# Kernel optimization log

Hardware: AMD Instinct MI355X
Metric: run time of the kernel (lower is better)

Reference implementation:

```python
import jax, jax.numpy as jnp
import numpy as np

DIM = 512
N = 1024
DIM_HEAD = 64
HEADS = 8
BATCH = 8
SCALE = DIM_HEAD ** -0.5


def setup_inputs() -> dict:
    key = jax.random.key(0)
    ks = jax.random.split(key, 9)
    s = 0.02
    return {
        "x": jax.random.normal(ks[0], (BATCH, N, DIM), dtype=jnp.float32),
        "w_qkv": jax.random.normal(ks[1], (3 * DIM, DIM), dtype=jnp.float32) * s,
        "b_qkv": jax.random.normal(ks[2], (3 * DIM,), dtype=jnp.float32) * s,
        "wq": jax.random.normal(ks[3], (N, DIM_HEAD), dtype=jnp.float32) * s,
        "bq": jax.random.normal(ks[4], (N,), dtype=jnp.float32) * s,
        "wk": jax.random.normal(ks[5], (N, DIM_HEAD), dtype=jnp.float32) * s,
        "bk": jax.random.normal(ks[6], (N,), dtype=jnp.float32) * s,
        "w_out": jax.random.normal(ks[7], (DIM, DIM), dtype=jnp.float32) * s,
        "b_out": jax.random.normal(ks[8], (DIM,), dtype=jnp.float32) * s,
    }


def _split_heads(t):
    # [b, n, h*d] -> [b, h, n, d]
    b, n, _ = t.shape
    return t.reshape(b, n, HEADS, DIM_HEAD).transpose(0, 2, 1, 3)


def reference(x, w_qkv, b_qkv, wq, bq, wk, bk, w_out, b_out):
    # fused QKV projection: [b, n, 3*dim]
    qkv = x @ w_qkv.T + b_qkv
    qo, ko, vo = jnp.split(qkv, 3, axis=-1)
    q, k, v = _split_heads(qo), _split_heads(ko), _split_heads(vo)  # [b,h,n,d]

    # additive-attention stage 1: A = softmax(Wq(q) * scale) over last dim
    A = jax.nn.softmax((jnp.einsum('bhnd,md->bhnm', q, wq) + bq) * SCALE, axis=-1)  # [b,h,n,n]
    q_global = jnp.sum(jnp.einsum('bhnm,bhmd->bhnd', A, q), axis=-1, keepdims=True)  # [b,h,n,1]
    p = q_global * k  # [b,h,n,d]

    # stage 2
    B = jax.nn.softmax((jnp.einsum('bhnd,md->bhnm', p, wk) + bk) * SCALE, axis=-1)  # [b,h,n,n]
    k_global = jnp.sum(jnp.einsum('bhnm,bhmd->bhnd', B, p), axis=-1, keepdims=True)  # [b,h,n,1]

    u = (k_global * v).transpose(0, 2, 1, 3).reshape(x.shape[0], N, DIM)  # [b,n,dim]
    out = u @ w_out.T + b_out + qo
    return out
```

## Files before the change

kernel.cpp:

```cpp
#include <hip/hip_runtime.h>


#define SCL 0.125f
#define SCL2 0.1803368801f
typedef unsigned short u16;
typedef __attribute__((ext_vector_type(8))) short short8;
typedef __attribute__((ext_vector_type(4))) float f32x4;

#define MFMA16(a, b, c) __builtin_amdgcn_mfma_f32_16x16x32_bf16((a), (b), (c), 0, 0, 0)

__device__ __forceinline__ float bf2f(u16 u) {
    union { unsigned int i; float f; } v; v.i = ((unsigned int)u) << 16; return v.f;
}
__device__ __forceinline__ u16 f2bf(float f) {
    union { float f; unsigned int i; } v; v.f = f;
    unsigned int x = v.i;
    return (u16)((x + 0x7FFFu + ((x >> 16) & 1u)) >> 16);
}

__device__ __forceinline__ void gload16(const u16* g, u16* l) {
    __builtin_amdgcn_global_load_lds(
        (__attribute__((address_space(1))) void*)(void*)g,
        (__attribute__((address_space(3))) void*)l, 16, 0, 0);
}

__global__ __launch_bounds__(256) void conv_kernel(
    const float* __restrict__ w_qkv, const float* __restrict__ w_out,
    const float* __restrict__ wq, const float* __restrict__ wk,
    const float* __restrict__ x, u16* __restrict__ wsb)
{
    const int idx = (blockIdx.x * 256 + threadIdx.x) * 4;
    const float* src; int off;
    if      (idx < 786432)  { src = w_qkv; off = idx; }
    else if (idx < 1048576) { src = w_out; off = idx - 786432; }
    else if (idx < 1114112) { src = wq;    off = idx - 1048576; }
    else if (idx < 1179648) { src = wk;    off = idx - 1114112; }
    else                    { src = x;     off = idx - 1179648; }
    float4 v = *(const float4*)(src + off);
    ushort4 o; o.x = f2bf(v.x); o.y = f2bf(v.y); o.z = f2bf(v.z); o.w = f2bf(v.w);
    *(ushort4*)(wsb + idx) = o;
}

#define MQK 0
#define MVU 1
#define MOUT 2

template <int MODE, int NCT>
__global__ __launch_bounds__(256) void gemm_k(
    const u16* __restrict__ Ab, int lda, int acol,
    const u16* __restrict__ Wb, const float* __restrict__ bias,
    const float* __restrict__ kg, const u16* __restrict__ qkws_ro,
    u16* __restrict__ qkws, float* __restrict__ outp,
    float* __restrict__ qsout, float* __restrict__ ksout)
{
    constexpr int BN = NCT * 16;
    constexpr int CST = BN + 8;
    constexpr int ASZ = 128 * 64;
    constexpr int BSZ = BN * 64;
    constexpr int HALF = ASZ + BSZ;
    constexpr int CELEM = 128 * CST;
    constexpr int SMSZ = (2 * HALF > HALF + CELEM) ? 2 * HALF : HALF + CELEM;
    __shared__ u16 sm[SMSZ];
    u16* const Cb = sm + HALF;

    const int t = threadIdx.x;
    const int w = t >> 6, lane = t & 63, s = lane & 15, quad = lane >> 4;
    const int sx = lane & 7;

    const int nwgy = gridDim.y;
    const int nwg = gridDim.x * nwgy;
    const int flat = blockIdx.y * gridDim.x + blockIdx.x;
    const int swz = (flat & 7) * (nwg >> 3) + (flat >> 3);
    const int by = swz % nwgy, bx = swz / nwgy;
    const int bm = bx * 128, jn0 = by * BN;

    const int r8 = lane >> 3;
    const int c8x = ((lane & 7) ^ r8) << 3;

    f32x4 acc[2][NCT];
#pragma unroll
    for (int i = 0; i < 2; ++i)
#pragma unroll
        for (int j = 0; j < NCT; ++j) acc[i][j] = (f32x4){0.f, 0.f, 0.f, 0.f};

    const u16* ga = Ab + (size_t)(bm + w * 32 + r8) * lda + acol + c8x;
    const u16* gb = Wb + (size_t)(jn0 + w * (NCT * 4) + r8) * 512 + c8x;

    auto stage = [&](int buf, int kt) {
        u16* la = sm + buf * HALF + (w * 32) * 64;
        u16* lb = sm + buf * HALF + ASZ + (w * (NCT * 4)) * 64;
#pragma unroll
        for (int j = 0; j < 4; ++j)
            gload16(ga + (size_t)j * 8 * lda + kt, la + j * 8 * 64);
#pragma unroll
        for (int j = 0; j < NCT / 2; ++j)
            gload16(gb + (size_t)j * 8 * 512 + kt, lb + j * 8 * 64);
    };
    auto compute = [&](int buf) {
        const u16* Ab_ = sm + buf * HALF;
        const u16* Bb_ = Ab_ + ASZ;
#pragma unroll
        for (int kk = 0; kk < 2; ++kk) {
            const int ca = ((kk * 4 + quad) ^ sx) << 3;
            short8 a0 = *(const short8*)&Ab_[(w * 32 + s) * 64 + ca];
            short8 a1 = *(const short8*)&Ab_[(w * 32 + 16 + s) * 64 + ca];
#pragma unroll
            for (int ct = 0; ct < NCT; ++ct) {
                short8 bf = *(const short8*)&Bb_[(ct * 16 + s) * 64 + ca];
                acc[0][ct] = MFMA16(a0, bf, acc[0][ct]);
                acc[1][ct] = MFMA16(a1, bf, acc[1][ct]);
            }
        }
    };

    stage(1, 0);
    __syncthreads();
#pragma unroll
    for (int it = 0; it < 7; ++it) {
        const int cur = 1 - (it & 1);
        stage(1 - cur, 64 * (it + 1));
        __builtin_amdgcn_sched_barrier(0);
        compute(cur);
        __syncthreads();
    }
    compute(0);

    if constexpr (MODE == MOUT) {
#pragma unroll
        for (int mt = 0; mt < 2; ++mt)
#pragma unroll
            for (int ct = 0; ct < NCT; ++ct) {
                const int jn = jn0 + ct * 16 + s;
#pragma unroll
                for (int r = 0; r < 4; ++r) {
                    const int row = bm + w * 32 + mt * 16 + quad * 4 + r;
                    outp[(size_t)row * 512 + jn] =
                        acc[mt][ct][r] + bias[jn] + bf2f(qkws_ro[(size_t)row * 1024 + jn]);
                }
            }
    } else {
        float rsum[2][NCT / 4][4];
        if constexpr (MODE == MQK) {
#pragma unroll
            for (int mt = 0; mt < 2; ++mt)
#pragma unroll
                for (int hg = 0; hg < NCT / 4; ++hg)
#pragma unroll
                    for (int r = 0; r < 4; ++r) rsum[mt][hg][r] = 0.f;
        }
        __syncthreads();
#pragma unroll
        for (int mt = 0; mt < 2; ++mt)
#pragma unroll
            for (int ct = 0; ct < NCT; ++ct) {
                const int jn = jn0 + ct * 16 + s;
                const float bj = bias[jn];
#pragma unroll
                for (int r = 0; r < 4; ++r) {
                    const int rowl = w * 32 + mt * 16 + quad * 4 + r;
                    float v = acc[mt][ct][r] + bj;
                    if constexpr (MODE == MVU) {
                        const int row = bm + rowl;
                        v *= kg[(((row >> 10) * 8 + (jn >> 6)) << 10) | (row & 1023)];
                    }
                    if constexpr (MODE == MQK) rsum[mt][ct >> 2][r] += v;
                    Cb[rowl * CST + ct * 16 + s] = f2bf(v);
                }
            }
        if constexpr (MODE == MQK) {
#pragma unroll
            for (int mt = 0; mt < 2; ++mt)
#pragma unroll
                for (int hg = 0; hg < NCT / 4; ++hg)
#pragma unroll
                    for (int r = 0; r < 4; ++r) {
                        float S = rsum[mt][hg][r];
                        S += __shfl_xor(S, 1);
                        S += __shfl_xor(S, 2);
                        S += __shfl_xor(S, 4);
                        S += __shfl_xor(S, 8);
                        if (s == 0) {
                            const int row = bm + w * 32 + mt * 16 + quad * 4 + r;
                            const int jj = jn0 + hg * 64;
                            float* dst = (jj < 512) ? qsout : ksout;
                            dst[((((row >> 10) << 3) | ((jj >> 6) & 7)) << 10) | (row & 1023)] = S;
                        }
                    }
        }
        __syncthreads();
        const int row = t >> 1, ch = (t & 1) * (NCT * 8);
        u16* dp = qkws + (size_t)(bm + row) * 1024 + (MODE == MVU ? 512 : 0) + jn0 + ch;
#pragma unroll
        for (int i = 0; i < NCT; ++i)
            *(uint4*)(dp + i * 8) = *(const uint4*)&Cb[row * CST + ch + i * 8];
    }
}

__global__ __launch_bounds__(256) void stage_soft(
    const u16* __restrict__ qkws, int qcol0,
    const u16* __restrict__ wmb, const float* __restrict__ biasv,
    const float* __restrict__ rowscale,
    const float* __restrict__ wv1, const float* __restrict__ wv2,
    float* __restrict__ outg)
{
    __shared__ float zr[4][64], wr[4][64];
    const int t = threadIdx.x;
    const int w = t >> 6, lane = t & 63, s = lane & 15, quad = lane >> 4;
    const int n0 = blockIdx.x * 64;
    const int bh = blockIdx.y, b = bh >> 3, h = bh & 7;

    short8 qa[4][2];
#pragma unroll
    for (int nt = 0; nt < 4; ++nt)
#pragma unroll
        for (int kk = 0; kk < 2; ++kk)
            qa[nt][kk] = *(const short8*)&qkws[
                (size_t)((b << 10) + n0 + nt * 16 + s) * 1024 + qcol0 + (h << 6) + kk * 32 + quad * 8];

    float rsS[4][4];
#pragma unroll
    for (int nt = 0; nt < 4; ++nt)
#pragma unroll
        for (int r = 0; r < 4; ++r)
            rsS[nt][r] = (rowscale ? rowscale[(bh << 10) + n0 + nt * 16 + quad * 4 + r] : 1.0f) * SCL2;

    float z[4][4] = {}, wa[4][4] = {};

    for (int mi = 0; mi < 16; ++mi) {
        const int mt = w * 256 + mi * 16;
        const u16* bp = wmb + (size_t)(mt + s) * 64 + quad * 8;
        short8 bf0 = *(const short8*)bp;
        short8 bf1 = *(const short8*)(bp + 32);
        const float bm2 = biasv[mt + s] * SCL2;
        float wv = wv1[(bh << 10) + mt + s];
        if (wv2) wv *= wv2[(bh << 10) + mt + s];
#pragma unroll
        for (int nt = 0; nt < 4; ++nt) {
            f32x4 a = (f32x4){0.f, 0.f, 0.f, 0.f};
            a = MFMA16(qa[nt][0], bf0, a);
            a = MFMA16(qa[nt][1], bf1, a);
#pragma unroll
            for (int r = 0; r < 4; ++r) {
                const float e = __builtin_amdgcn_exp2f(rsS[nt][r] * a[r] + bm2);
                z[nt][r] += e;
                wa[nt][r] += e * wv;
            }
        }
    }

#pragma unroll
    for (int nt = 0; nt < 4; ++nt)
#pragma unroll
        for (int r = 0; r < 4; ++r) {
            float Z = z[nt][r], W = wa[nt][r];
            for (int off = 1; off < 16; off <<= 1) {
                Z += __shfl_xor(Z, off);
                W += __shfl_xor(W, off);
            }
            if (s == 0) {
                zr[w][nt * 16 + quad * 4 + r] = Z;
                wr[w][nt * 16 + quad * 4 + r] = W;
            }
        }
    __syncthreads();
    if (t < 64) {
        float Z = zr[0][t] + zr[1][t] + zr[2][t] + zr[3][t];
        float W = wr[0][t] + wr[1][t] + wr[2][t] + wr[3][t];
        outg[(bh << 10) + n0 + t] = W / Z;
    }
}

extern "C" void kernel_launch(void* const* d_in, const int* in_sizes, int n_in,
                              void* d_out, int out_size, void* d_ws, size_t ws_size,
                              hipStream_t stream)
{
    const float* x     = (const float*)d_in[0];
    const float* w_qkv = (const float*)d_in[1];
    const float* b_qkv = (const float*)d_in[2];
    const float* wq    = (const float*)d_in[3];
    const float* bq    = (const float*)d_in[4];
    const float* wk    = (const float*)d_in[5];
    const float* bk    = (const float*)d_in[6];
    const float* w_out = (const float*)d_in[7];
    const float* b_out = (const float*)d_in[8];
    float* out = (float*)d_out;

    float* qs = (float*)d_ws;
    float* ks = qs + 65536;
    float* qg = ks + 65536;
    float* kg = qg + 65536;
    u16* wsb   = (u16*)(kg + 65536);
    u16* wqkvb = wsb;
    u16* woutb = wqkvb + 786432;
    u16* wqb   = woutb + 262144;
    u16* wkb   = wqb + 65536;
    u16* xb    = wkb + 65536;
    u16* qkws  = xb + 4194304;

    conv_kernel<<<5248, 256, 0, stream>>>(w_qkv, w_out, wq, wk, x, wsb);
    gemm_k<MQK, 8><<<dim3(64, 8), 256, 0, stream>>>(
        xb, 512, 0, wqkvb, b_qkv, nullptr, nullptr, qkws, nullptr, qs, ks);
    stage_soft<<<dim3(16, 64), 256, 0, stream>>>(
        qkws, 0, wqb, bq, nullptr, qs, nullptr, qg);
    stage_soft<<<dim3(16, 64), 256, 0, stream>>>(
        qkws, 512, wkb, bk, qg, qg, ks, kg);
    gemm_k<MVU, 4><<<dim3(64, 8), 256, 0, stream>>>(
        xb, 512, 0, wqkvb + (size_t)1024 * 512, b_qkv + 1024, kg, nullptr, qkws, nullptr,
        nullptr, nullptr);
    gemm_k<MOUT, 4><<<dim3(64, 8), 256, 0, stream>>>(
        qkws, 1024, 512, woutb, b_out, nullptr, qkws, nullptr, out, nullptr, nullptr);
}
```

Measured before the change: 183.1 us.

## Fuse GEMM and softmax stages into one cooperative persistent kernel with grid syncs

Replaces the five launches after conversion with a single cooperative mega-kernel of 512 blocks that runs each stage in turn, separated by grid-wide barriers. The softmax stages loop over 1024 work units per block pair. Stage variants are specialized at compile time so the runtime null checks on rowscale and wv2 go away. The aim is to remove launch gaps and tail effects between small kernels, at the cost of grid-sync overhead and requiring 2 blocks per CU of residency. If the cooperative launch fails, the code falls back to the old multi-kernel path.

After: 432.3 us. 2.36x slower.

```diff
diff --git a/kernel.cpp b/kernel.cpp
--- a/kernel.cpp
+++ b/kernel.cpp
@@ -1,7 +1,8 @@
 #include <hip/hip_runtime.h>
-
-
-#define SCL 0.125f
+#include <hip/hip_cooperative_groups.h>
+namespace cg = cooperative_groups;
+
+
 #define SCL2 0.1803368801f
 typedef unsigned short u16;
 typedef __attribute__((ext_vector_type(8))) short short8;
@@ -46,7 +47,8 @@
 #define MOUT 2
 
 template <int MODE, int NCT>
-__global__ __launch_bounds__(256) void gemm_k(
+__device__ __forceinline__ void gemm_body(
+    u16* sm, int flat,
     const u16* __restrict__ Ab, int lda, int acol,
     const u16* __restrict__ Wb, const float* __restrict__ bias,
     const float* __restrict__ kg, const u16* __restrict__ qkws_ro,
@@ -58,20 +60,14 @@
     constexpr int ASZ = 128 * 64;
     constexpr int BSZ = BN * 64;
     constexpr int HALF = ASZ + BSZ;
-    constexpr int CELEM = 128 * CST;
-    constexpr int SMSZ = (2 * HALF > HALF + CELEM) ? 2 * HALF : HALF + CELEM;
-    __shared__ u16 sm[SMSZ];
     u16* const Cb = sm + HALF;
 
     const int t = threadIdx.x;
     const int w = t >> 6, lane = t & 63, s = lane & 15, quad = lane >> 4;
     const int sx = lane & 7;
 
-    const int nwgy = gridDim.y;
-    const int nwg = gridDim.x * nwgy;
-    const int flat = blockIdx.y * gridDim.x + blockIdx.x;
-    const int swz = (flat & 7) * (nwg >> 3) + (flat >> 3);
-    const int by = swz % nwgy, bx = swz / nwgy;
+    const int swz = (flat & 7) * 64 + (flat >> 3);
+    const int by = swz & 7, bx = swz >> 3;
     const int bm = bx * 128, jn0 = by * BN;
 
     const int r8 = lane >> 3;
@@ -196,18 +192,21 @@
     }
 }
 
-__global__ __launch_bounds__(256) void stage_soft(
+template <int STG>
+__device__ __forceinline__ void stage_body(
+    u16* smraw, int u,
     const u16* __restrict__ qkws, int qcol0,
     const u16* __restrict__ wmb, const float* __restrict__ biasv,
     const float* __restrict__ rowscale,
     const float* __restrict__ wv1, const float* __restrict__ wv2,
     float* __restrict__ outg)
 {
-    __shared__ float zr[4][64], wr[4][64];
+    float* zr = (float*)smraw;
+    float* wr = zr + 256;
     const int t = threadIdx.x;
     const int w = t >> 6, lane = t & 63, s = lane & 15, quad = lane >> 4;
-    const int n0 = blockIdx.x * 64;
-    const int bh = blockIdx.y, b = bh >> 3, h = bh & 7;
+    const int n0 = (u & 15) * 64;
+    const int bh = u >> 4, b = bh >> 3, h = bh & 7;
 
     short8 qa[4][2];
 #pragma unroll
@@ -221,8 +220,12 @@
 #pragma unroll
     for (int nt = 0; nt < 4; ++nt)
 #pragma unroll
-        for (int r = 0; r < 4; ++r)
-            rsS[nt][r] = (rowscale ? rowscale[(bh << 10) + n0 + nt * 16 + quad * 4 + r] : 1.0f) * SCL2;
+        for (int r = 0; r < 4; ++r) {
+            if constexpr (STG == 2)
+                rsS[nt][r] = rowscale[(bh << 10) + n0 + nt * 16 + quad * 4 + r] * SCL2;
+            else
+                rsS[nt][r] = SCL2;
+        }
 
     float z[4][4] = {}, wa[4][4] = {};
 
@@ -233,7 +236,7 @@
         short8 bf1 = *(const short8*)(bp + 32);
         const float bm2 = biasv[mt + s] * SCL2;
         float wv = wv1[(bh << 10) + mt + s];
-        if (wv2) wv *= wv2[(bh << 10) + mt + s];
+        if constexpr (STG == 2) wv *= wv2[(bh << 10) + mt + s];
 #pragma unroll
         for (int nt = 0; nt < 4; ++nt) {
             f32x4 a = (f32x4){0.f, 0.f, 0.f, 0.f};
@@ -258,16 +261,70 @@
                 W += __shfl_xor(W, off);
             }
             if (s == 0) {
-                zr[w][nt * 16 + quad * 4 + r] = Z;
-                wr[w][nt * 16 + quad * 4 + r] = W;
+                zr[w * 64 + nt * 16 + quad * 4 + r] = Z;
+                wr[w * 64 + nt * 16 + quad * 4 + r] = W;
             }
         }
     __syncthreads();
     if (t < 64) {
-        float Z = zr[0][t] + zr[1][t] + zr[2][t] + zr[3][t];
-        float W = wr[0][t] + wr[1][t] + wr[2][t] + wr[3][t];
+        float Z = zr[t] + zr[64 + t] + zr[128 + t] + zr[192 + t];
+        float W = wr[t] + wr[64 + t] + wr[128 + t] + wr[192 + t];
         outg[(bh << 10) + n0 + t] = W / Z;
     }
+}
+
+__global__ __launch_bounds__(256, 2) void mega_kernel(
+    const u16* xb, const u16* wqkvb, const u16* woutb,
+    const u16* wqb, const u16* wkb,
+    const float* b_qkv, const float* bq, const float* bk, const float* b_out,
+    float* qs, float* ks, float* qg, float* kg, u16* qkws, float* out)
+{
+    __shared__ u16 sm[33792];
+    cg::grid_group grid = cg::this_grid();
+
+    gemm_body<MQK, 8>(sm, (int)blockIdx.x, xb, 512, 0, wqkvb, b_qkv,
+                      nullptr, nullptr, qkws, nullptr, qs, ks);
+    grid.sync();
+#pragma unroll
+    for (int u = blockIdx.x; u < 1024; u += 512) {
+        stage_body<1>(sm, u, qkws, 0, wqb, bq, nullptr, qs, nullptr, qg);
+        __syncthreads();
+    }
+    grid.sync();
+#pragma unroll
+    for (int u = blockIdx.x; u < 1024; u += 512) {
+        stage_body<2>(sm, u, qkws, 512, wkb, bk, qg, qg, ks, kg);
+        __syncthreads();
+    }
+    grid.sync();
+    gemm_body<MVU, 4>(sm, (int)blockIdx.x, xb, 512, 0,
+                      wqkvb + (size_t)1024 * 512, b_qkv + 1024, kg,
+                      nullptr, qkws, nullptr, nullptr, nullptr);
+    grid.sync();
+    gemm_body<MOUT, 4>(sm, (int)blockIdx.x, qkws, 1024, 512, woutb, b_out,
+                       nullptr, qkws, nullptr, out, nullptr, nullptr);
+}
+
+template <int MODE, int NCT>
+__global__ __launch_bounds__(256) void gemm_k(
+    const u16* Ab, int lda, int acol, const u16* Wb, const float* bias,
+    const float* kg, const u16* qkws_ro, u16* qkws, float* outp,
+    float* qsout, float* ksout)
+{
+    constexpr int SMSZ = (NCT == 8) ? 33792 : 24576;
+    __shared__ u16 sm[SMSZ];
+    gemm_body<MODE, NCT>(sm, (int)(blockIdx.y * gridDim.x + blockIdx.x),
+                         Ab, lda, acol, Wb, bias, kg, qkws_ro, qkws, outp, qsout, ksout);
+}
+
+template <int STG>
+__global__ __launch_bounds__(256) void stage_soft_w(
+    const u16* qkws, int qcol0, const u16* wmb, const float* biasv,
+    const float* rowscale, const float* wv1, const float* wv2, float* outg)
+{
+    __shared__ float zw[512];
+    stage_body<STG>((u16*)zw, (int)(blockIdx.y * 16 + blockIdx.x),
+                    qkws, qcol0, wmb, biasv, rowscale, wv1, wv2, outg);
 }
 
 extern "C" void kernel_launch(void* const* d_in, const int* in_sizes, int n_in,
@@ -298,15 +355,26 @@
     u16* qkws  = xb + 4194304;
 
     conv_kernel<<<5248, 256, 0, stream>>>(w_qkv, w_out, wq, wk, x, wsb);
-    gemm_k<MQK, 8><<<dim3(64, 8), 256, 0, stream>>>(
-        xb, 512, 0, wqkvb, b_qkv, nullptr, nullptr, qkws, nullptr, qs, ks);
-    stage_soft<<<dim3(16, 64), 256, 0, stream>>>(
-        qkws, 0, wqb, bq, nullptr, qs, nullptr, qg);
-    stage_soft<<<dim3(16, 64), 256, 0, stream>>>(
-        qkws, 512, wkb, bk, qg, qg, ks, kg);
-    gemm_k<MVU, 4><<<dim3(64, 8), 256, 0, stream>>>(
-        xb, 512, 0, wqkvb + (size_t)1024 * 512, b_qkv + 1024, kg, nullptr, qkws, nullptr,
-        nullptr, nullptr);
-    gemm_k<MOUT, 4><<<dim3(64, 8), 256, 0, stream>>>(
-        qkws, 1024, 512, woutb, b_out, nullptr, qkws, nullptr, out, nullptr, nullptr);
-}
+
+    const u16* xb_c = xb; const u16* wqkvb_c = wqkvb; const u16* woutb_c = woutb;
+    const u16* wqb_c = wqb; const u16* wkb_c = wkb;
+    void* args[] = {
+        (void*)&xb_c, (void*)&wqkvb_c, (void*)&woutb_c, (void*)&wqb_c, (void*)&wkb_c,
+        (void*)&b_qkv, (void*)&bq, (void*)&bk, (void*)&b_out,
+        (void*)&qs, (void*)&ks, (void*)&qg, (void*)&kg, (void*)&qkws, (void*)&out };
+    hipError_t e = hipLaunchCooperativeKernel(
+        (const void*)mega_kernel, dim3(512), dim3(256), args, 0u, stream);
+    if (e != hipSuccess) {
+        gemm_k<MQK, 8><<<dim3(64, 8), 256, 0, stream>>>(
+            xb, 512, 0, wqkvb, b_qkv, nullptr, nullptr, qkws, nullptr, qs, ks);
+        stage_soft_w<1><<<dim3(16, 64), 256, 0, stream>>>(
+            qkws, 0, wqb, bq, nullptr, qs, nullptr, qg);
+        stage_soft_w<2><<<dim3(16, 64), 256, 0, stream>>>(
+            qkws, 512, wkb, bk, qg, qg, ks, kg);
+        gemm_k<MVU, 4><<<dim3(64, 8), 256, 0, stream>>>(
+            xb, 512, 0, wqkvb + (size_t)1024 * 512, b_qkv + 1024, kg, nullptr, qkws,
+            nullptr, nullptr, nullptr);
+        gemm_k<MOUT, 4><<<dim3(64, 8), 256, 0, stream>>>(
+            qkws, 1024, 512, woutb, b_out, nullptr, qkws, nullptr, out, nullptr, nullptr);
+    }
+}
```

## Restructure softmax stage into LDS-tiled double-buffered GEMM with swizzled block order

Applied to the files above, without the earlier changes.

The fused softmax-reduction kernel is rewritten so each block handles 128 rows, with each wave owning 32 rows and sweeping all 1024 columns. Wq/Wk column tiles are staged through swizzled, double-buffered LDS using global_load_lds, where before every wave loaded its own B fragments from global memory. The block index is also swizzled for L2 locality, and the cross-wave LDS reduction is gone. The aim is less redundant global traffic and better overlap of loads with MFMA and exp work. In exchange, the grid has fewer blocks (512 vs 1024), per-chunk __syncthreads are added, and each wave now carries less MFMA work per B fragment.

Result: slower. 531.3 us (+190.2%).

```diff
diff --git a/kernel.cpp b/kernel.cpp
--- a/kernel.cpp
+++ b/kernel.cpp
@@ -1,7 +1,6 @@
 #include <hip/hip_runtime.h>
 
 
-#define SCL 0.125f
 #define SCL2 0.1803368801f
 typedef unsigned short u16;
 typedef __attribute__((ext_vector_type(8))) short short8;
@@ -196,78 +195,117 @@
     }
 }
 
-__global__ __launch_bounds__(256) void stage_soft(
+template <int STG>
+__global__ __launch_bounds__(256) void stage_gemm(
     const u16* __restrict__ qkws, int qcol0,
     const u16* __restrict__ wmb, const float* __restrict__ biasv,
     const float* __restrict__ rowscale,
     const float* __restrict__ wv1, const float* __restrict__ wv2,
     float* __restrict__ outg)
 {
-    __shared__ float zr[4][64], wr[4][64];
+    __shared__ u16 sm[24576];
+    u16* const As = sm;
+
     const int t = threadIdx.x;
     const int w = t >> 6, lane = t & 63, s = lane & 15, quad = lane >> 4;
-    const int n0 = blockIdx.x * 64;
-    const int bh = blockIdx.y, b = bh >> 3, h = bh & 7;
-
-    short8 qa[4][2];
-#pragma unroll
-    for (int nt = 0; nt < 4; ++nt)
+    const int sx = lane & 7;
+    const int r8 = lane >> 3;
+    const int c8x = ((lane & 7) ^ r8) << 3;
+
+    const int flat = blockIdx.y * gridDim.x + blockIdx.x;
+    const int swz = (flat & 7) * 64 + (flat >> 3);
+    const int h = swz & 7, bx = swz >> 3;
+    const int bm = bx * 128;
+    const int bh = ((bm >> 10) << 3) + h;
+    const int n0 = bm & 1023;
+
+    const u16* gA = qkws + (size_t)(bm + w * 32 + r8) * 1024 + qcol0 + (h << 6) + c8x;
+    const u16* gB = wmb + (size_t)(w * 32 + r8) * 64 + c8x;
+
+    auto stageB = [&](int buf, int c) {
+        u16* lb = sm + 8192 + buf * 8192 + (w * 32) * 64;
+        const u16* g = gB + (size_t)c * 128 * 64;
+#pragma unroll
+        for (int j = 0; j < 4; ++j)
+            gload16(g + (size_t)j * 8 * 64, lb + j * 8 * 64);
+    };
+
+#pragma unroll
+    for (int j = 0; j < 4; ++j)
+        gload16(gA + (size_t)j * 8 * 1024, As + (w * 32 + j * 8) * 64);
+    stageB(1, 0);
+    __syncthreads();
+
+    short8 a[2][2];
+#pragma unroll
+    for (int nt = 0; nt < 2; ++nt)
 #pragma unroll
         for (int kk = 0; kk < 2; ++kk)
-            qa[nt][kk] = *(const short8*)&qkws[
-                (size_t)((b << 10) + n0 + nt * 16 + s) * 1024 + qcol0 + (h << 6) + kk * 32 + quad * 8];
-
-    float rsS[4][4];
-#pragma unroll
-    for (int nt = 0; nt < 4; ++nt)
-#pragma unroll
-        for (int r = 0; r < 4; ++r)
-            rsS[nt][r] = (rowscale ? rowscale[(bh << 10) + n0 + nt * 16 + quad * 4 + r] : 1.0f) * SCL2;
-
-    float z[4][4] = {}, wa[4][4] = {};
-
-    for (int mi = 0; mi < 16; ++mi) {
-        const int mt = w * 256 + mi * 16;
-        const u16* bp = wmb + (size_t)(mt + s) * 64 + quad * 8;
-        short8 bf0 = *(const short8*)bp;
-        short8 bf1 = *(const short8*)(bp + 32);
-        const float bm2 = biasv[mt + s] * SCL2;
-        float wv = wv1[(bh << 10) + mt + s];
-        if (wv2) wv *= wv2[(bh << 10) + mt + s];
-#pragma unroll
-        for (int nt = 0; nt < 4; ++nt) {
-            f32x4 a = (f32x4){0.f, 0.f, 0.f, 0.f};
-            a = MFMA16(qa[nt][0], bf0, a);
-            a = MFMA16(qa[nt][1], bf1, a);
-#pragma unroll
-            for (int r = 0; r < 4; ++r) {
-                const float e = __builtin_amdgcn_exp2f(rsS[nt][r] * a[r] + bm2);
-                z[nt][r] += e;
-                wa[nt][r] += e * wv;
-            }
-        }
+            a[nt][kk] = *(const short8*)&As[(w * 32 + nt * 16 + s) * 64 + (((kk * 4 + quad) ^ sx) << 3)];
+
+    float rsf[2][4];
+#pragma unroll
+    for (int nt = 0; nt < 2; ++nt)
+#pragma unroll
+        for (int r = 0; r < 4; ++r) {
+            if constexpr (STG == 2)
+                rsf[nt][r] = rowscale[(bh << 10) + n0 + w * 32 + nt * 16 + quad * 4 + r] * SCL2;
+            else
+                rsf[nt][r] = SCL2;
+        }
+
+    float z[2][4] = {}, wacc[2][4] = {};
+
+#pragma unroll
+    for (int c = 0; c < 8; ++c) {
+        const int cur = 1 - (c & 1);
+        if (c < 7) stageB(1 - cur, c + 1);
+        __builtin_amdgcn_sched_barrier(0);
+
+        const int mb = c * 128;
+        float bmv[8], wvv[8];
+#pragma unroll
+        for (int ct = 0; ct < 8; ++ct) {
+            const int m = mb + ct * 16 + s;
+            bmv[ct] = biasv[m] * SCL2;
+            float wv = wv1[(bh << 10) + m];
+            if constexpr (STG == 2) wv *= wv2[(bh << 10) + m];
+            wvv[ct] = wv;
+        }
+
+        const u16* Bb = sm + 8192 + cur * 8192;
+#pragma unroll
+        for (int ct = 0; ct < 8; ++ct) {
+            const short8 b0 = *(const short8*)&Bb[(ct * 16 + s) * 64 + ((quad ^ sx) << 3)];
+            const short8 b1 = *(const short8*)&Bb[(ct * 16 + s) * 64 + (((4 + quad) ^ sx) << 3)];
+#pragma unroll
+            for (int nt = 0; nt < 2; ++nt) {
+                f32x4 acc = (f32x4){0.f, 0.f, 0.f, 0.f};
+                acc = MFMA16(a[nt][0], b0, acc);
+                acc = MFMA16(a[nt][1], b1, acc);
+#pragma unroll
+                for (int r = 0; r < 4; ++r) {
+                    const float e = __builtin_amdgcn_exp2f(rsf[nt][r] * acc[r] + bmv[ct]);
+                    z[nt][r] += e;
+                    wacc[nt][r] += e * wvv[ct];
+                }
+            }
+        }
+        __syncthreads();
     }
 
 #pragma unroll
-    for (int nt = 0; nt < 4; ++nt)
+    for (int nt = 0; nt < 2; ++nt)
 #pragma unroll
         for (int r = 0; r < 4; ++r) {
-            float Z = z[nt][r], W = wa[nt][r];
+            float Z = z[nt][r], W = wacc[nt][r];
             for (int off = 1; off < 16; off <<= 1) {
                 Z += __shfl_xor(Z, off);
                 W += __shfl_xor(W, off);
             }
-            if (s == 0) {
-                zr[w][nt * 16 + quad * 4 + r] = Z;
-                wr[w][nt * 16 + quad * 4 + r] = W;
-            }
-        }
-    __syncthreads();
-    if (t < 64) {
-        float Z = zr[0][t] + zr[1][t] + zr[2][t] + zr[3][t];
-        float W = wr[0][t] + wr[1][t] + wr[2][t] + wr[3][t];
-        outg[(bh << 10) + n0 + t] = W / Z;
-    }
+            if (s == 0)
+                outg[(bh << 10) + n0 + w * 32 + nt * 16 + quad * 4 + r] = W / Z;
+        }
 }
 
 extern "C" void kernel_launch(void* const* d_in, const int* in_sizes, int n_in,
@@ -300,13 +338,13 @@
     conv_kernel<<<5248, 256, 0, stream>>>(w_qkv, w_out, wq, wk, x, wsb);
     gemm_k<MQK, 8><<<dim3(64, 8), 256, 0, stream>>>(
         xb, 512, 0, wqkvb, b_qkv, nullptr, nullptr, qkws, nullptr, qs, ks);
-    stage_soft<<<dim3(16, 64), 256, 0, stream>>>(
+    stage_gemm<1><<<dim3(64, 8), 256, 0, stream>>>(
         qkws, 0, wqb, bq, nullptr, qs, nullptr, qg);
-    stage_soft<<<dim3(16, 64), 256, 0, stream>>>(
+    stage_gemm<2><<<dim3(64, 8), 256, 0, stream>>>(
         qkws, 512, wkb, bk, qg, qg, ks, kg);
     gemm_k<MVU, 4><<<dim3(64, 8), 256, 0, stream>>>(
-        xb, 512, 0, wqkvb + (size_t)1024 * 512, b_qkv + 1024, kg, nullptr, qkws, nullptr,
-        nullptr, nullptr);
+        xb, 512, 0, wqkvb + (size_t)1024 * 512, b_qkv + 1024, kg, nullptr, qkws,
+        nullptr, nullptr, nullptr);
     gemm_k<MOUT, 4><<<dim3(64, 8), 256, 0, stream>>>(
         qkws, 1024, 512, woutb, b_out, nullptr, qkws, nullptr, out, nullptr, nullptr);
 }
```
